# Kernel optimization log

Hardware: AMD Instinct MI355X
Metric: run time of the kernel (lower is better)

Reference implementation:

```python
import jax, jax.numpy as jnp
import numpy as np
from jax import lax

DW_THR = 4.0
PW_THR = 1e-3
EPS = 1e-5


def _bn(x, gamma, beta, mean, var):
    # inference-mode BatchNorm2d over channel axis 1
    inv = gamma * lax.rsqrt(var + EPS)
    return x * inv[None, :, None, None] + (beta - mean * inv)[None, :, None, None]


def _prune(x, thr):
    # zero each (batch, channel) feature map whose max-abs < thr
    maxabs = jnp.max(jnp.abs(x), axis=(2, 3), keepdims=True)  # [B,C,1,1]
    return jnp.where(maxabs < thr, jnp.zeros((), x.dtype), x)


def setup_inputs() -> dict:
    key = jax.random.key(0)
    ks = jax.random.split(key, 8)
    B, Cin, Cout, H, W = 32, 256, 512, 56, 56
    x = jax.random.normal(ks[0], (B, Cin, H, W), jnp.float32)
    dw_w = jax.random.normal(ks[1], (Cin, 1, 3, 3), jnp.float32) * (1.0 / 3.0)
    dw_b = jax.random.normal(ks[2], (Cin,), jnp.float32) * 0.1
    bn1_gamma = jnp.ones((Cin,), jnp.float32)
    bn1_beta = jnp.zeros((Cin,), jnp.float32)
    bn1_mean = jnp.zeros((Cin,), jnp.float32)
    bn1_var = jnp.ones((Cin,), jnp.float32)
    pw_w = jax.random.normal(ks[3], (Cout, Cin), jnp.float32) * (1.0 / np.sqrt(Cin))
    pw_b = jax.random.normal(ks[4], (Cout,), jnp.float32) * 0.1
    bn2_gamma = jnp.ones((Cout,), jnp.float32)
    bn2_beta = jnp.zeros((Cout,), jnp.float32)
    bn2_mean = jnp.zeros((Cout,), jnp.float32)
    bn2_var = jnp.ones((Cout,), jnp.float32)
    return dict(x=x, dw_w=dw_w, dw_b=dw_b,
                bn1_gamma=bn1_gamma, bn1_beta=bn1_beta, bn1_mean=bn1_mean, bn1_var=bn1_var,
                pw_w=pw_w, pw_b=pw_b,
                bn2_gamma=bn2_gamma, bn2_beta=bn2_beta, bn2_mean=bn2_mean, bn2_var=bn2_var)


def reference(x, dw_w, dw_b, bn1_gamma, bn1_beta, bn1_mean, bn1_var,
              pw_w, pw_b, bn2_gamma, bn2_beta, bn2_mean, bn2_var):
    Cin = x.shape[1]
    # depthwise 3x3 conv, padding=1, groups=Cin
    y = lax.conv_general_dilated(
        x, dw_w, window_strides=(1, 1), padding=((1, 1), (1, 1)),
        feature_group_count=Cin,
        dimension_numbers=('NCHW', 'OIHW', 'NCHW'))
    y = y + dw_b[None, :, None, None]
    y = jax.nn.relu(_bn(y, bn1_gamma, bn1_beta, bn1_mean, bn1_var))
    y = _prune(y, DW_THR)
    # pointwise 1x1 conv == channel GEMM
    z = jnp.einsum('bchw,oc->bohw', y, pw_w) + pw_b[None, :, None, None]
    z = jax.nn.relu(_bn(z, bn2_gamma, bn2_beta, bn2_mean, bn2_var))
    z = _prune(z, PW_THR)
    return z
```

## Files before the change

kernel.cpp:

```cpp
#include <hip/hip_runtime.h>
#include <hip/hip_bf16.h>

#define EPSV 1e-5f
#define DW_THR 4.0f
#define PW_THR 1e-3f

static constexpr int BB = 32, CIN = 256, COUT = 512, HH = 56, WW = 56, HW = HH * WW;

typedef __attribute__((ext_vector_type(8))) short bf16x8;
typedef __attribute__((ext_vector_type(4))) float f32x4;
typedef __attribute__((ext_vector_type(8))) unsigned short u16x8;

__device__ __forceinline__ void glds16(const void* g, void* l) {
    __builtin_amdgcn_global_load_lds((const __attribute__((address_space(1))) void*)g,
                                     (__attribute__((address_space(3))) void*)l, 16, 0, 0);
}

__global__ __launch_bounds__(256) void dw_kernel(
    const float* __restrict__ x, const float* __restrict__ dw_w, const float* __restrict__ dw_b,
    const float* __restrict__ g1, const float* __restrict__ b1,
    const float* __restrict__ m1, const float* __restrict__ v1,
    __hip_bfloat16* __restrict__ y, int* __restrict__ flags)
{
    const int blk = blockIdx.x;
    const int c   = blk & (CIN - 1);
    const int tid = threadIdx.x;

    __shared__ float xs[58 * 68];
    for (int i = tid; i < 58 * 17; i += 256) *(f32x4*)&xs[i * 4] = (f32x4){0.f, 0.f, 0.f, 0.f};
    __syncthreads();
    const float* xp = x + (size_t)blk * HW;
    for (int i = tid; i < 56 * 14; i += 256) {
        int r = i / 14, q = i - r * 14;
        *(f32x4*)&xs[(r + 1) * 68 + 4 + q * 4] = *(const f32x4*)(xp + i * 4);
    }

    float w[9];
#pragma unroll
    for (int k = 0; k < 9; k++) w[k] = dw_w[c * 9 + k];
    const float inv = g1[c] * rsqrtf(v1[c] + EPSV);
    const float sh  = (dw_b[c] - m1[c]) * inv + b1[c];
    __syncthreads();

    float vals[14];
    float mx = 0.f;
    const int row = tid >> 2, strip = tid & 3;
    if (tid < 224) {
        const float* base = xs + row * 68 + strip * 14 + 4;
        float a0 = base[-1],       a1 = base[0];
        float b0 = base[68 - 1],   b1v = base[68];
        float c0 = base[136 - 1],  c1 = base[136];
#pragma unroll
        for (int i = 0; i < 14; i++) {
            const float a2 = base[i + 1];
            const float b2 = base[68 + i + 1];
            const float c2 = base[136 + i + 1];
            float s;
            s = a0 * w[0];
            s = fmaf(a1, w[1], s); s = fmaf(a2, w[2], s);
            s = fmaf(b0, w[3], s); s = fmaf(b1v, w[4], s); s = fmaf(b2, w[5], s);
            s = fmaf(c0, w[6], s); s = fmaf(c1, w[7], s); s = fmaf(c2, w[8], s);
            const float val = fmaxf(fmaf(s, inv, sh), 0.f);
            vals[i] = val;
            mx = fmaxf(mx, val);
            a0 = a1; a1 = a2; b0 = b1v; b1v = b2; c0 = c1; c1 = c2;
        }
    }

    for (int off = 32; off > 0; off >>= 1) mx = fmaxf(mx, __shfl_xor(mx, off));
    __shared__ float redw[4];
    if ((tid & 63) == 0) redw[tid >> 6] = mx;
    __syncthreads();
    const float bmax = fmaxf(fmaxf(redw[0], redw[1]), fmaxf(redw[2], redw[3]));
    const int survive = (bmax >= DW_THR) ? 1 : 0;
    if (tid == 0) flags[blk] = survive;
    if (survive && tid < 224) {
        unsigned short* yp = (unsigned short*)(y + (size_t)blk * HW) + row * 56 + strip * 14;
#pragma unroll
        for (int i = 0; i < 7; i++) {
            ushort2 pk;
            pk.x = __bfloat16_as_ushort(__float2bfloat16(vals[2 * i]));
            pk.y = __bfloat16_as_ushort(__float2bfloat16(vals[2 * i + 1]));
            *(ushort2*)(yp + 2 * i) = pk;
        }
    }
}

__global__ __launch_bounds__(256) void fold_kernel(
    const float* __restrict__ pw_w, const float* __restrict__ pw_b,
    const float* __restrict__ g2, const float* __restrict__ b2,
    const float* __restrict__ m2, const float* __restrict__ v2,
    __hip_bfloat16* __restrict__ Wf, float* __restrict__ cterm)
{
    const int o = blockIdx.x, t = threadIdx.x;
    const float inv = g2[o] * rsqrtf(v2[o] + EPSV);
    Wf[o * CIN + t] = __float2bfloat16(pw_w[o * CIN + t] * inv);
    if (t == 0) cterm[o] = (pw_b[o] - m2[o]) * inv + b2[o];
}

__global__ __launch_bounds__(256) void transpose_kernel(
    const __hip_bfloat16* __restrict__ y, const int* __restrict__ flags,
    __hip_bfloat16* __restrict__ yT)
{
    const int blk = blockIdx.x;
    const int nt = blk % 49;
    const int rem = blk / 49;
    const int ct = rem & 3;
    const int b  = rem >> 2;
    const int t = threadIdx.x;

    __shared__ unsigned short ts[64][68];
    __shared__ int fl[64];
    if (t < 64) fl[t] = flags[b * CIN + ct * 64 + t];
    __syncthreads();

    const unsigned short* yp = (const unsigned short*)y + ((size_t)b * CIN + ct * 64) * HW + nt * 64;
#pragma unroll
    for (int k = 0; k < 4; k++) {
        int u = t + k * 256;
        int row = u >> 4, cu = u & 15;
        ushort4 v = make_ushort4(0, 0, 0, 0);
        if (fl[row]) v = *(const ushort4*)(yp + (size_t)row * HW + cu * 4);
        *(ushort4*)(&ts[row][cu * 4]) = v;
    }
    __syncthreads();

    unsigned short* yTp = (unsigned short*)yT + ((size_t)b * HW + (size_t)nt * 64) * CIN + ct * 64;
    const int n = t >> 2, l4 = t & 3;
#pragma unroll
    for (int h = 0; h < 2; h++) {
        const int c8 = (l4 + h * 4) * 8;
        u16x8 v;
#pragma unroll
        for (int j = 0; j < 8; j++) v[j] = ts[c8 + j][n];
        *(u16x8*)(yTp + (size_t)n * CIN + c8) = v;
    }
}

__global__ __launch_bounds__(256) void gemm_kernel(
    const __hip_bfloat16* __restrict__ Wf_, const __hip_bfloat16* __restrict__ yT_,
    const float* __restrict__ cterm, float* __restrict__ out, float* __restrict__ pmax)
{
    const int orig = blockIdx.x;
    const int blk  = (orig & 7) * 400 + (orig >> 3);
    const int b    = blk / 100;
    const int rem  = blk % 100;
    const int mt = rem / 25, nt = rem % 25;
    const int tid = threadIdx.x, l = tid & 63, wid = tid >> 6;
    const int wm = wid >> 1, wn = wid & 1;
    const int lr = l & 15, lk = l >> 4;
    const int o0 = mt * 128, n0 = nt * 128;

    __shared__ unsigned short Al[128 * 32];
    __shared__ unsigned short Bl[128 * 32];

    const short* W = (const short*)Wf_;
    const short* Y = (const short*)yT_ + (size_t)b * HW * CIN;

    const int kch   = (((l & 3) ^ ((l >> 3) & 3)) << 3);
    const int rowA  = o0 + 32 * wid + (l >> 2);
    const short* asrc0 = W + (size_t)rowA * CIN + kch;
    const short* asrc1 = W + (size_t)(rowA + 16) * CIN + kch;
    const int rowB  = n0 + 32 * wid + (l >> 2);
    const short* bsrc0 = Y + (size_t)rowB * CIN + kch;
    const short* bsrc1 = Y + (size_t)(rowB + 16) * CIN + kch;

    f32x4 acc[4][4];
#pragma unroll
    for (int nr = 0; nr < 4; nr++)
#pragma unroll
        for (int mr = 0; mr < 4; mr++) acc[nr][mr] = (f32x4){0.f, 0.f, 0.f, 0.f};

#pragma unroll
    for (int t = 0; t < 8; t++) {
        const int k0 = t * 32;
        glds16(asrc0 + k0, (void*)(&Al[(2 * wid) * 512]));
        glds16(asrc1 + k0, (void*)(&Al[(2 * wid + 1) * 512]));
        glds16(bsrc0 + k0, (void*)(&Bl[(2 * wid) * 512]));
        glds16(bsrc1 + k0, (void*)(&Bl[(2 * wid + 1) * 512]));
        __syncthreads();

        bf16x8 a[4], bb[4];
#pragma unroll
        for (int mr = 0; mr < 4; mr++) {
            const int r = wm * 64 + mr * 16 + lr;
            a[mr] = *(const bf16x8*)((const char*)Al + r * 64 + ((lk ^ ((r >> 1) & 3)) << 4));
        }
#pragma unroll
        for (int nr = 0; nr < 4; nr++) {
            const int r = wn * 64 + nr * 16 + lr;
            bb[nr] = *(const bf16x8*)((const char*)Bl + r * 64 + ((lk ^ ((r >> 1) & 3)) << 4));
        }
#pragma unroll
        for (int nr = 0; nr < 4; nr++)
#pragma unroll
            for (int mr = 0; mr < 4; mr++)
                acc[nr][mr] = __builtin_amdgcn_mfma_f32_16x16x32_bf16(bb[nr], a[mr], acc[nr][mr], 0, 0, 0);
        __syncthreads();
    }

    float ct[4], om[4];
#pragma unroll
    for (int mr = 0; mr < 4; mr++) {
        ct[mr] = cterm[o0 + wm * 64 + mr * 16 + lr];
        om[mr] = 0.f;
    }
    const int nb0 = n0 + wn * 64;
#pragma unroll
    for (int nr = 0; nr < 4; nr++) {
        const int n4 = nb0 + nr * 16 + lk * 4;
        if (n4 < HW) {
#pragma unroll
            for (int mr = 0; mr < 4; mr++) {
                const int o = o0 + wm * 64 + mr * 16 + lr;
                f32x4 z;
                z[0] = fmaxf(acc[nr][mr][0] + ct[mr], 0.f);
                z[1] = fmaxf(acc[nr][mr][1] + ct[mr], 0.f);
                z[2] = fmaxf(acc[nr][mr][2] + ct[mr], 0.f);
                z[3] = fmaxf(acc[nr][mr][3] + ct[mr], 0.f);
                __builtin_nontemporal_store(z, (f32x4*)(out + ((size_t)b * COUT + o) * HW + n4));
                om[mr] = fmaxf(om[mr], fmaxf(fmaxf(z[0], z[1]), fmaxf(z[2], z[3])));
            }
        }
    }
#pragma unroll
    for (int mr = 0; mr < 4; mr++) {
        om[mr] = fmaxf(om[mr], __shfl_xor(om[mr], 16));
        om[mr] = fmaxf(om[mr], __shfl_xor(om[mr], 32));
    }
    if (l < 16) {
#pragma unroll
        for (int mr = 0; mr < 4; mr++) {
            const int o = o0 + wm * 64 + mr * 16 + lr;
            pmax[(size_t)(b * COUT + o) * 50 + nt * 2 + wn] = om[mr];
        }
    }
}

__global__ __launch_bounds__(64) void fixup_kernel(const float* __restrict__ pmax, float* __restrict__ out)
{
    const int blk = blockIdx.x;
    const int b = blk >> 9, o = blk & 511;
    const int t = threadIdx.x;
    float m = (t < 50) ? pmax[(size_t)(b * COUT + o) * 50 + t] : 0.f;
#pragma unroll
    for (int d = 1; d < 64; d <<= 1) m = fmaxf(m, __shfl_xor(m, d));
    if (m < PW_THR) {
        float* p = out + ((size_t)b * COUT + o) * HW;
        for (int n = t; n < HW; n += 64) p[n] = 0.f;
    }
}

extern "C" void kernel_launch(void* const* d_in, const int* in_sizes, int n_in,
                              void* d_out, int out_size, void* d_ws, size_t ws_size,
                              hipStream_t stream)
{
    const float* x    = (const float*)d_in[0];
    const float* dw_w = (const float*)d_in[1];
    const float* dw_b = (const float*)d_in[2];
    const float* g1   = (const float*)d_in[3];
    const float* b1   = (const float*)d_in[4];
    const float* m1   = (const float*)d_in[5];
    const float* v1   = (const float*)d_in[6];
    const float* pw_w = (const float*)d_in[7];
    const float* pw_b = (const float*)d_in[8];
    const float* g2   = (const float*)d_in[9];
    const float* b2   = (const float*)d_in[10];
    const float* m2   = (const float*)d_in[11];
    const float* v2   = (const float*)d_in[12];
    float* out = (float*)d_out;

    char* ws = (char*)d_ws;
    size_t off = 0;
    __hip_bfloat16* y  = (__hip_bfloat16*)(ws + off); off += (size_t)BB * CIN * HW * 2;
    __hip_bfloat16* yT = (__hip_bfloat16*)(ws + off); off += (size_t)BB * HW * CIN * 2 + 65536;
    int*   flags = (int*)(ws + off);   off += (size_t)BB * CIN * 4;
    __hip_bfloat16* Wf = (__hip_bfloat16*)(ws + off); off += (size_t)COUT * CIN * 2;
    float* cterm = (float*)(ws + off); off += (size_t)COUT * 4;
    float* pmax  = (float*)(ws + off); off += (size_t)BB * COUT * 50 * 4;

    fold_kernel<<<COUT, CIN, 0, stream>>>(pw_w, pw_b, g2, b2, m2, v2, Wf, cterm);
    dw_kernel<<<BB * CIN, 256, 0, stream>>>(x, dw_w, dw_b, g1, b1, m1, v1, y, flags);
    transpose_kernel<<<BB * 4 * 49, 256, 0, stream>>>(y, flags, yT);
    gemm_kernel<<<BB * 4 * 25, 256, 0, stream>>>(Wf, yT, cterm, out, pmax);
    fixup_kernel<<<BB * COUT, 64, 0, stream>>>(pmax, out);
}
```

Before: 120.7 us.

## Fuse transpose into GEMM by loading channel-major activations directly into LDS

Removes the separate transpose kernel and its bf16 yT buffer. The GEMM now reads the channel-major depthwise output directly, applies the per-channel prune flags while loading, and packs channel pairs into a padded LDS tile for the B operand. This saves a full write and read of the intermediate activations and one launch. In exchange the B loads go through registers instead of async global-to-LDS copies, use a padded layout that may cause bank conflicts, and the last N tile reads past HW, which is covered by the extra workspace padding.

```diff
diff --git a/kernel.cpp b/kernel.cpp
--- a/kernel.cpp
+++ b/kernel.cpp
@@ -98,48 +98,10 @@
     if (t == 0) cterm[o] = (pw_b[o] - m2[o]) * inv + b2[o];
 }
 
-__global__ __launch_bounds__(256) void transpose_kernel(
-    const __hip_bfloat16* __restrict__ y, const int* __restrict__ flags,
-    __hip_bfloat16* __restrict__ yT)
-{
-    const int blk = blockIdx.x;
-    const int nt = blk % 49;
-    const int rem = blk / 49;
-    const int ct = rem & 3;
-    const int b  = rem >> 2;
-    const int t = threadIdx.x;
-
-    __shared__ unsigned short ts[64][68];
-    __shared__ int fl[64];
-    if (t < 64) fl[t] = flags[b * CIN + ct * 64 + t];
-    __syncthreads();
-
-    const unsigned short* yp = (const unsigned short*)y + ((size_t)b * CIN + ct * 64) * HW + nt * 64;
-#pragma unroll
-    for (int k = 0; k < 4; k++) {
-        int u = t + k * 256;
-        int row = u >> 4, cu = u & 15;
-        ushort4 v = make_ushort4(0, 0, 0, 0);
-        if (fl[row]) v = *(const ushort4*)(yp + (size_t)row * HW + cu * 4);
-        *(ushort4*)(&ts[row][cu * 4]) = v;
-    }
-    __syncthreads();
-
-    unsigned short* yTp = (unsigned short*)yT + ((size_t)b * HW + (size_t)nt * 64) * CIN + ct * 64;
-    const int n = t >> 2, l4 = t & 3;
-#pragma unroll
-    for (int h = 0; h < 2; h++) {
-        const int c8 = (l4 + h * 4) * 8;
-        u16x8 v;
-#pragma unroll
-        for (int j = 0; j < 8; j++) v[j] = ts[c8 + j][n];
-        *(u16x8*)(yTp + (size_t)n * CIN + c8) = v;
-    }
-}
-
 __global__ __launch_bounds__(256) void gemm_kernel(
-    const __hip_bfloat16* __restrict__ Wf_, const __hip_bfloat16* __restrict__ yT_,
-    const float* __restrict__ cterm, float* __restrict__ out, float* __restrict__ pmax)
+    const __hip_bfloat16* __restrict__ Wf_, const __hip_bfloat16* __restrict__ y_,
+    const int* __restrict__ flags, const float* __restrict__ cterm,
+    float* __restrict__ out, float* __restrict__ pmax)
 {
     const int orig = blockIdx.x;
     const int blk  = (orig & 7) * 400 + (orig >> 3);
@@ -152,32 +114,46 @@
     const int o0 = mt * 128, n0 = nt * 128;
 
     __shared__ unsigned short Al[128 * 32];
-    __shared__ unsigned short Bl[128 * 32];
+    __shared__ unsigned short Bl[128 * 34];
+    __shared__ int fl[CIN];
+
+    fl[tid] = flags[b * CIN + tid];
 
     const short* W = (const short*)Wf_;
-    const short* Y = (const short*)yT_ + (size_t)b * HW * CIN;
+    const unsigned short* Y = (const unsigned short*)y_ + (size_t)b * CIN * HW;
 
     const int kch   = (((l & 3) ^ ((l >> 3) & 3)) << 3);
     const int rowA  = o0 + 32 * wid + (l >> 2);
     const short* asrc0 = W + (size_t)rowA * CIN + kch;
     const short* asrc1 = W + (size_t)(rowA + 16) * CIN + kch;
-    const int rowB  = n0 + 32 * wid + (l >> 2);
-    const short* bsrc0 = Y + (size_t)rowB * CIN + kch;
-    const short* bsrc1 = Y + (size_t)(rowB + 16) * CIN + kch;
+
+    const int cp = tid & 15, ng = tid >> 4;
+    const int nB = n0 + ng * 8;
+    const int nloc = ng * 8;
 
     f32x4 acc[4][4];
 #pragma unroll
     for (int nr = 0; nr < 4; nr++)
 #pragma unroll
         for (int mr = 0; mr < 4; mr++) acc[nr][mr] = (f32x4){0.f, 0.f, 0.f, 0.f};
+
+    __syncthreads();
 
 #pragma unroll
     for (int t = 0; t < 8; t++) {
         const int k0 = t * 32;
         glds16(asrc0 + k0, (void*)(&Al[(2 * wid) * 512]));
         glds16(asrc1 + k0, (void*)(&Al[(2 * wid + 1) * 512]));
-        glds16(bsrc0 + k0, (void*)(&Bl[(2 * wid) * 512]));
-        glds16(bsrc1 + k0, (void*)(&Bl[(2 * wid + 1) * 512]));
+
+        const int c0 = k0 + cp * 2;
+        u16x8 v0 = (u16x8){0,0,0,0,0,0,0,0}, v1 = (u16x8){0,0,0,0,0,0,0,0};
+        if (fl[c0])     v0 = *(const u16x8*)(Y + (size_t)c0 * HW + nB);
+        if (fl[c0 + 1]) v1 = *(const u16x8*)(Y + (size_t)(c0 + 1) * HW + nB);
+#pragma unroll
+        for (int j = 0; j < 8; j++) {
+            const unsigned pk = (unsigned)v0[j] | ((unsigned)v1[j] << 16);
+            *(unsigned*)((char*)Bl + (nloc + j) * 68 + cp * 4) = pk;
+        }
         __syncthreads();
 
         bf16x8 a[4], bb[4];
@@ -189,7 +165,7 @@
 #pragma unroll
         for (int nr = 0; nr < 4; nr++) {
             const int r = wn * 64 + nr * 16 + lr;
-            bb[nr] = *(const bf16x8*)((const char*)Bl + r * 64 + ((lk ^ ((r >> 1) & 3)) << 4));
+            bb[nr] = *(const bf16x8*)((const char*)Bl + r * 68 + lk * 16);
         }
 #pragma unroll
         for (int nr = 0; nr < 4; nr++)
@@ -272,8 +248,7 @@
 
     char* ws = (char*)d_ws;
     size_t off = 0;
-    __hip_bfloat16* y  = (__hip_bfloat16*)(ws + off); off += (size_t)BB * CIN * HW * 2;
-    __hip_bfloat16* yT = (__hip_bfloat16*)(ws + off); off += (size_t)BB * HW * CIN * 2 + 65536;
+    __hip_bfloat16* y  = (__hip_bfloat16*)(ws + off); off += (size_t)BB * CIN * HW * 2 + 256;
     int*   flags = (int*)(ws + off);   off += (size_t)BB * CIN * 4;
     __hip_bfloat16* Wf = (__hip_bfloat16*)(ws + off); off += (size_t)COUT * CIN * 2;
     float* cterm = (float*)(ws + off); off += (size_t)COUT * 4;
@@ -281,7 +256,6 @@
 
     fold_kernel<<<COUT, CIN, 0, stream>>>(pw_w, pw_b, g2, b2, m2, v2, Wf, cterm);
     dw_kernel<<<BB * CIN, 256, 0, stream>>>(x, dw_w, dw_b, g1, b1, m1, v1, y, flags);
-    transpose_kernel<<<BB * 4 * 49, 256, 0, stream>>>(y, flags, yT);
-    gemm_kernel<<<BB * 4 * 25, 256, 0, stream>>>(Wf, yT, cterm, out, pmax);
+    gemm_kernel<<<BB * 4 * 25, 256, 0, stream>>>(Wf, y, flags, cterm, out, pmax);
     fixup_kernel<<<BB * COUT, 64, 0, stream>>>(pmax, out);
 }
```

Measured after the change: 114.0 us. -5.6%, faster.
